# Performance work log

Hardware: AMD Instinct MI355X
Metric: run time of the kernel (lower is better)

## Reference

```python
import jax, jax.numpy as jnp
import numpy as np


def setup_inputs() -> dict:
    key = jax.random.key(0)
    k1, k2 = jax.random.split(key, 2)
    B, K, N, Fdim = 32, 8, 2048, 64
    regime_probs = jax.random.uniform(k1, (B, K), dtype=jnp.float32)
    factor_loadings = jax.random.normal(k2, (K, N, Fdim), dtype=jnp.float32)
    specific_risk = jnp.ones((K, N), dtype=jnp.float32)
    return {
        "regime_probs": regime_probs,
        "factor_loadings": factor_loadings,
        "specific_risk": specific_risk,
    }


def reference(regime_probs, factor_loadings, specific_risk):
    # Handle [B, K, T] -> take last time step (as in original)
    if regime_probs.ndim == 3:
        regime_probs = regime_probs[:, :, -1]
    K, N, _ = factor_loadings.shape
    # Per-regime covariance: F_k F_k^T + diag(specific_risk_k^2)  -> [K, N, N]
    cov_k = jnp.einsum("knf,kmf->knm", factor_loadings, factor_loadings)
    eye = jnp.eye(N, dtype=cov_k.dtype)
    cov_k = cov_k + eye[None, :, :] * (specific_risk ** 2)[:, :, None]
    # Regime-weighted mixture per batch element -> [B, N, N]
    return jnp.einsum("bk,knm->bnm", regime_probs, cov_k)
```

## Files before the change

kernel.cpp:

```cpp
#include <hip/hip_runtime.h>

#define NDIM 2048
#define FDIM 64
#define KDIM 8
#define BDIM 32
#define TN   16
#define TM   128
#define BFROW 72
#define PROW  132
#define PLANES 4
#define NTILE 4

typedef __attribute__((ext_vector_type(8))) short short8;
typedef __attribute__((ext_vector_type(4))) float f32x4;

static __device__ __forceinline__ unsigned short f2bf(float x) {
    unsigned u = __float_as_uint(x);
    return (unsigned short)((u + 0x7fffu + ((u >> 16) & 1u)) >> 16);
}

__global__ __launch_bounds__(256, 2) void rfm_fused_mfma(
    const float* __restrict__ p, const float* __restrict__ L,
    const float* __restrict__ sr, float* __restrict__ out)
{
    __shared__ float pl[BDIM * KDIM];
    __shared__ __align__(16) char smem[PLANES * TN * PROW * 4];

    unsigned short* const An = (unsigned short*)smem;
    unsigned short* const Am = An + TN * BFROW;
    float* const Parr0 = (float*)smem;
    float* const Parr1 = Parr0 + TN * PROW;
    float* const Parr2 = Parr1 + TN * PROW;
    float* const Parr3 = Parr2 + TN * PROW;

    const int t  = threadIdx.x;
    const int lane = t & 63;
    const int w   = t >> 6;
    const int l15 = lane & 15;
    const int l4  = lane >> 4;

    pl[t] = p[t];

    const int sa_row = t >> 4;
    const int sa_fc  = (t & 15) << 2;

    #pragma unroll 1
    for (int tt = 0; tt < NTILE; ++tt) {
        const int tile = (int)blockIdx.x + tt * 512;
        const int m0 = (tile & 15) * TM;
        const int n0 = (tile >> 4) * TN;

        f32x4 acc[KDIM][2];
        #pragma unroll
        for (int k = 0; k < KDIM; ++k)
            #pragma unroll
            for (int j = 0; j < 2; ++j) acc[k][j] = (f32x4){0.f, 0.f, 0.f, 0.f};

        float4 pva;
        float4 pvb[8];
        {
            const float* Lk = L;
            pva = *(const float4*)&Lk[(size_t)(n0 + sa_row) * FDIM + sa_fc];
            #pragma unroll
            for (int r = 0; r < 8; ++r) {
                const int idx = t + r * 256;
                pvb[r] = *(const float4*)
                    &Lk[(size_t)(m0 + (idx >> 4)) * FDIM + ((idx & 15) << 2)];
            }
        }

        #pragma unroll
        for (int k = 0; k < KDIM; ++k) {
            {
                ushort4 ua;
                ua.x = f2bf(pva.x); ua.y = f2bf(pva.y);
                ua.z = f2bf(pva.z); ua.w = f2bf(pva.w);
                *(ushort4*)&An[sa_row * BFROW + sa_fc] = ua;
            }
            #pragma unroll
            for (int r = 0; r < 8; ++r) {
                const int idx = t + r * 256;
                ushort4 ub;
                ub.x = f2bf(pvb[r].x); ub.y = f2bf(pvb[r].y);
                ub.z = f2bf(pvb[r].z); ub.w = f2bf(pvb[r].w);
                *(ushort4*)&Am[(idx >> 4) * BFROW + ((idx & 15) << 2)] = ub;
            }
            __syncthreads();

            if (k + 1 < KDIM) {
                const float* Lk1 = L + (size_t)(k + 1) * (NDIM * FDIM);
                pva = *(const float4*)&Lk1[(size_t)(n0 + sa_row) * FDIM + sa_fc];
                #pragma unroll
                for (int r = 0; r < 8; ++r) {
                    const int idx = t + r * 256;
                    pvb[r] = *(const float4*)
                        &Lk1[(size_t)(m0 + (idx >> 4)) * FDIM + ((idx & 15) << 2)];
                }
            }

            short8 af[2], bv[2][2];
            #pragma unroll
            for (int s = 0; s < 2; ++s)
                af[s] = *(const short8*)&An[l15 * BFROW + s * 32 + l4 * 8];
            #pragma unroll
            for (int j = 0; j < 2; ++j)
                #pragma unroll
                for (int s = 0; s < 2; ++s)
                    bv[j][s] = *(const short8*)
                        &Am[(w * 32 + j * 16 + l15) * BFROW + s * 32 + l4 * 8];
            #pragma unroll
            for (int j = 0; j < 2; ++j)
                #pragma unroll
                for (int s = 0; s < 2; ++s)
                    acc[k][j] = __builtin_amdgcn_mfma_f32_16x16x32_bf16(
                        af[s], bv[j][s], acc[k][j], 0, 0, 0);
            __syncthreads();
        }

        #pragma unroll
        for (int j = 0; j < 2; ++j)
            #pragma unroll
            for (int reg = 0; reg < 4; ++reg) {
                const int gn = n0 + l4 * 4 + reg;
                const int gm = m0 + w * 32 + j * 16 + l15;
                if (gn == gm) {
                    #pragma unroll
                    for (int k = 0; k < KDIM; ++k) {
                        const float q = sr[k * NDIM + gn];
                        acc[k][j][reg] += q * q;
                    }
                }
            }

        const size_t NN = (size_t)NDIM * NDIM;
        float* const Parr[PLANES] = { Parr0, Parr1, Parr2, Parr3 };
        const int scr = l4 * 4;
        const int scc = w * 32 + l15;
        const int rbrow = t >> 5;
        const int rbc4  = (t & 31) * 4;
        float* const obase = out + (size_t)n0 * NDIM + m0 + rbc4;

        #pragma unroll 1
        for (int b = 0; b < BDIM; b += PLANES) {
            #pragma unroll
            for (int u = 0; u < PLANES; ++u) {
                float pb[KDIM];
                #pragma unroll
                for (int k = 0; k < KDIM; ++k) pb[k] = pl[(b + u) * KDIM + k];
                float* const Pu = Parr[u];
                #pragma unroll
                for (int j = 0; j < 2; ++j)
                    #pragma unroll
                    for (int reg = 0; reg < 4; ++reg) {
                        float v = 0.0f;
                        #pragma unroll
                        for (int k = 0; k < KDIM; ++k)
                            v += pb[k] * acc[k][j][reg];
                        Pu[(scr + reg) * PROW + scc + j * 16] = v;
                    }
            }
            asm volatile("s_waitcnt lgkmcnt(0)" ::: "memory");
            __builtin_amdgcn_s_barrier();
            __builtin_amdgcn_sched_barrier(0);

            #pragma unroll
            for (int u = 0; u < PLANES; ++u) {
                const float* const Pu = Parr[u];
                const size_t boff = (size_t)(b + u) * NN;
                #pragma unroll
                for (int rr = 0; rr < 2; ++rr) {
                    const int row = rbrow + 8 * rr;
                    const f32x4 wv = *(const f32x4*)&Pu[row * PROW + rbc4];
                    __builtin_nontemporal_store(wv,
                        (f32x4*)(obase + boff + (size_t)row * NDIM));
                }
            }
            asm volatile("s_waitcnt lgkmcnt(0)" ::: "memory");
            __builtin_amdgcn_s_barrier();
            __builtin_amdgcn_sched_barrier(0);
        }
    }
}

extern "C" void kernel_launch(void* const* d_in, const int* in_sizes, int n_in,
                              void* d_out, int out_size, void* d_ws, size_t ws_size,
                              hipStream_t stream)
{
    const float* p  = (const float*)d_in[0];
    const float* L  = (const float*)d_in[1];
    const float* sr = (const float*)d_in[2];
    float* out = (float*)d_out;

    hipLaunchKernelGGL(rfm_fused_mfma, dim3(512), dim3(256), 0, stream,
                       p, L, sr, out);
}
```

Measured before the change: 108.7 us.

## Double-buffer LDS operand tiles and prefetch next tile's loadings across epilogue

Splits the bf16 operand staging area into two LDS buffers alternating by regime, so each step needs only one barrier instead of two. It also prefetches the first regime's loadings for the next tile during the last regime step, so the global load latency overlaps the mixing and store epilogue. A barrier before the epilogue protects the aliased plane buffers. The cost is extra LDS use and register pressure carried across the epilogue, and the output store phase likely dominates runtime anyway.

```diff
diff --git a/kernel.cpp b/kernel.cpp
--- a/kernel.cpp
+++ b/kernel.cpp
@@ -24,10 +24,12 @@
     const float* __restrict__ sr, float* __restrict__ out)
 {
     __shared__ float pl[BDIM * KDIM];
-    __shared__ __align__(16) char smem[PLANES * TN * PROW * 4];
-
-    unsigned short* const An = (unsigned short*)smem;
-    unsigned short* const Am = An + TN * BFROW;
+    __shared__ __align__(16) char smem[2 * (TN + TM) * BFROW * 2];
+
+    unsigned short* const An0 = (unsigned short*)smem;
+    unsigned short* const Am0 = An0 + TN * BFROW;
+    unsigned short* const An1 = Am0 + TM * BFROW;
+    unsigned short* const Am1 = An1 + TN * BFROW;
     float* const Parr0 = (float*)smem;
     float* const Parr1 = Parr0 + TN * PROW;
     float* const Parr2 = Parr1 + TN * PROW;
@@ -43,10 +45,25 @@
 
     const int sa_row = t >> 4;
     const int sa_fc  = (t & 15) << 2;
+    const int bid = (int)blockIdx.x;
+
+    float4 pva;
+    float4 pvb[8];
+    {
+        const int m0p = (bid & 15) * TM;
+        const int n0p = (bid >> 4) * TN;
+        pva = *(const float4*)&L[(size_t)(n0p + sa_row) * FDIM + sa_fc];
+        #pragma unroll
+        for (int r = 0; r < 8; ++r) {
+            const int idx = t + r * 256;
+            pvb[r] = *(const float4*)
+                &L[(size_t)(m0p + (idx >> 4)) * FDIM + ((idx & 15) << 2)];
+        }
+    }
 
     #pragma unroll 1
     for (int tt = 0; tt < NTILE; ++tt) {
-        const int tile = (int)blockIdx.x + tt * 512;
+        const int tile = bid + tt * 512;
         const int m0 = (tile & 15) * TM;
         const int n0 = (tile >> 4) * TN;
 
@@ -56,26 +73,16 @@
             #pragma unroll
             for (int j = 0; j < 2; ++j) acc[k][j] = (f32x4){0.f, 0.f, 0.f, 0.f};
 
-        float4 pva;
-        float4 pvb[8];
-        {
-            const float* Lk = L;
-            pva = *(const float4*)&Lk[(size_t)(n0 + sa_row) * FDIM + sa_fc];
-            #pragma unroll
-            for (int r = 0; r < 8; ++r) {
-                const int idx = t + r * 256;
-                pvb[r] = *(const float4*)
-                    &Lk[(size_t)(m0 + (idx >> 4)) * FDIM + ((idx & 15) << 2)];
-            }
-        }
-
         #pragma unroll
         for (int k = 0; k < KDIM; ++k) {
+            unsigned short* const Anb = (k & 1) ? An1 : An0;
+            unsigned short* const Amb = (k & 1) ? Am1 : Am0;
+
             {
                 ushort4 ua;
                 ua.x = f2bf(pva.x); ua.y = f2bf(pva.y);
                 ua.z = f2bf(pva.z); ua.w = f2bf(pva.w);
-                *(ushort4*)&An[sa_row * BFROW + sa_fc] = ua;
+                *(ushort4*)&Anb[sa_row * BFROW + sa_fc] = ua;
             }
             #pragma unroll
             for (int r = 0; r < 8; ++r) {
@@ -83,9 +90,8 @@
                 ushort4 ub;
                 ub.x = f2bf(pvb[r].x); ub.y = f2bf(pvb[r].y);
                 ub.z = f2bf(pvb[r].z); ub.w = f2bf(pvb[r].w);
-                *(ushort4*)&Am[(idx >> 4) * BFROW + ((idx & 15) << 2)] = ub;
-            }
-            __syncthreads();
+                *(ushort4*)&Amb[(idx >> 4) * BFROW + ((idx & 15) << 2)] = ub;
+            }
 
             if (k + 1 < KDIM) {
                 const float* Lk1 = L + (size_t)(k + 1) * (NDIM * FDIM);
@@ -96,25 +102,39 @@
                     pvb[r] = *(const float4*)
                         &Lk1[(size_t)(m0 + (idx >> 4)) * FDIM + ((idx & 15) << 2)];
                 }
-            }
+            } else if (tt + 1 < NTILE) {
+                const int tile2 = bid + (tt + 1) * 512;
+                const int m0b = (tile2 & 15) * TM;
+                const int n0b = (tile2 >> 4) * TN;
+                pva = *(const float4*)&L[(size_t)(n0b + sa_row) * FDIM + sa_fc];
+                #pragma unroll
+                for (int r = 0; r < 8; ++r) {
+                    const int idx = t + r * 256;
+                    pvb[r] = *(const float4*)
+                        &L[(size_t)(m0b + (idx >> 4)) * FDIM + ((idx & 15) << 2)];
+                }
+            }
+
+            asm volatile("s_waitcnt lgkmcnt(0)" ::: "memory");
+            __builtin_amdgcn_s_barrier();
+            __builtin_amdgcn_sched_barrier(0);
 
             short8 af[2], bv[2][2];
             #pragma unroll
             for (int s = 0; s < 2; ++s)
-                af[s] = *(const short8*)&An[l15 * BFROW + s * 32 + l4 * 8];
+                af[s] = *(const short8*)&Anb[l15 * BFROW + s * 32 + l4 * 8];
             #pragma unroll
             for (int j = 0; j < 2; ++j)
                 #pragma unroll
                 for (int s = 0; s < 2; ++s)
                     bv[j][s] = *(const short8*)
-                        &Am[(w * 32 + j * 16 + l15) * BFROW + s * 32 + l4 * 8];
+                        &Amb[(w * 32 + j * 16 + l15) * BFROW + s * 32 + l4 * 8];
             #pragma unroll
             for (int j = 0; j < 2; ++j)
                 #pragma unroll
                 for (int s = 0; s < 2; ++s)
                     acc[k][j] = __builtin_amdgcn_mfma_f32_16x16x32_bf16(
                         af[s], bv[j][s], acc[k][j], 0, 0, 0);
-            __syncthreads();
         }
 
         #pragma unroll
@@ -132,6 +152,10 @@
                 }
             }
 
+        asm volatile("s_waitcnt lgkmcnt(0)" ::: "memory");
+        __builtin_amdgcn_s_barrier();
+        __builtin_amdgcn_sched_barrier(0);
+
         const size_t NN = (size_t)NDIM * NDIM;
         float* const Parr[PLANES] = { Parr0, Parr1, Parr2, Parr3 };
         const int scr = l4 * 4;
```

Measured after the change: 145.5 us. +33.9%, slower.
